# Performance work log

Hardware: AMD Instinct MI355X
Metric: run time of the kernel (lower is better)

The kernel has to match this reference:

```python
import jax, jax.numpy as jnp
import numpy as np

T = 0.2          # temperature
W = 0.1          # loss weight
BIG = 2 ** 30    # sentinel label for masked-out samples


def setup_inputs() -> dict:
    key = jax.random.key(0)
    k1, k2, k3, k4 = jax.random.split(key, 4)
    bs, C, Gn, S = 32, 128, 256, 16
    grouped_features = jax.random.normal(k1, (bs, C, Gn, S), dtype=jnp.float32)
    # instance labels in [-1, 8): -1 = background
    proposal_instance_mask = jax.random.randint(k2, (bs, Gn, S), -1, 8, dtype=jnp.int32)
    # seed indices with duplicates possible (range 40 over 16 samples)
    grouped_indices = jax.random.randint(k3, (bs, Gn, S), 0, 40, dtype=jnp.int32)
    context_compen = jax.random.normal(k4, (1, C), dtype=jnp.float32)
    return {
        "proposal_instance_mask": proposal_instance_mask,
        "grouped_features": grouped_features,
        "grouped_indices": grouped_indices,
        "context_compen": context_compen,
    }


def _group_loss(feat, idx, lab, ctx):
    # feat: [S, C], idx: [S], lab: [S], ctx: [C]
    # NOTE: sum_{a,b} f_a . g_b / (n_f * n_g) == mean(f) . mean(g), so the
    # original tiny-mm contrastive loss reduces to pairwise dots of per-instance means.
    S, C = feat.shape
    pos = jnp.arange(S)
    # unique count of seed indices -> truncate to first u samples (as in torch code)
    si = jnp.sort(idx)
    u = 1 + jnp.sum(si[1:] != si[:-1])
    valid = pos < u
    lab_m = jnp.where(valid, lab, BIG)
    # per-group unique labels (sorted), jit-friendly
    sl = jnp.sort(lab_m)
    new = jnp.concatenate([jnp.ones((1,), bool), sl[1:] != sl[:-1]])
    cid = jnp.cumsum(new) - 1                      # compact id of each sorted label
    uniq = jnp.full((S,), BIG, sl.dtype).at[cid].set(sl)
    n_labels = jnp.sum(new & (sl != BIG))          # number of distinct valid labels
    has_bg = uniq[0] == -1                         # -1 sorts first if present
    # per-instance mean features via segment scatter-add
    comp = jnp.searchsorted(uniq, lab_m)           # sample -> compact instance slot
    sums = jnp.zeros((S, C), feat.dtype).at[comp].add(jnp.where(valid[:, None], feat, 0.0))
    cnts = jnp.zeros((S,), feat.dtype).at[comp].add(valid.astype(feat.dtype))
    means = sums / jnp.maximum(cnts, 1.0)[:, None]
    hb = has_bg.astype(jnp.int32)
    fg_count = n_labels - hb
    inst_num = fg_count + 1                        # bg slot always present
    # row 0 = bg mean (or context_compen if no bg), rows 1.. = fg means
    gidx = jnp.clip(pos + hb - 1, 0, S - 1)
    M = means[gidx]
    M = M.at[0].set(jnp.where(has_bg, M[0], ctx))
    inst_valid = pos < inst_num
    sim = (M @ M.T) / T                            # [S, S] tiny matmul of means
    sim_m = jnp.where(inst_valid[None, :], sim, -jnp.inf)
    lse = jax.scipy.special.logsumexp(sim_m, axis=1)
    li = lse - jnp.diagonal(sim)                   # -log(pos/(pos+neg)) per fg row
    fg_mask = inst_valid & (pos >= 1)
    gl = jnp.sum(jnp.where(fg_mask, li, 0.0)) / jnp.maximum(inst_num - 1, 1).astype(feat.dtype)
    return gl, fg_count >= 1


def reference(proposal_instance_mask, grouped_features, grouped_indices, context_compen):
    bs, C, Gn, S = grouped_features.shape
    feats = grouped_features.transpose(0, 2, 3, 1).reshape(-1, S, C)  # [G, S, C]
    idxs = grouped_indices.reshape(-1, S)
    labs = proposal_instance_mask.reshape(-1, S)
    ctx = context_compen[0]
    gl, gv = jax.vmap(lambda f, i, l: _group_loss(f, i, l, ctx))(feats, idxs, labs)
    gvf = gv.astype(gl.dtype)
    return jnp.sum(gl * gvf) / jnp.sum(gvf) * W
```

## Files before the change

### kernel.cpp

```cpp
#include <hip/hip_runtime.h>

#define GQ   8192
#define WPB  2
#define MROW 132
#define SLICE 1280

__global__ __launch_bounds__(64 * WPB, 6) void group_loss_kernel(
    const int*   __restrict__ labs,
    const float* __restrict__ feats,
    const int*   __restrict__ idxs,
    const float* __restrict__ ctx,
    float2* __restrict__ ws)
{
    __shared__ float SH[WPB * SLICE];

    const int l  = threadIdx.x & 63;
    const int wu = threadIdx.x >> 6;
    float* MM   = SH + wu * SLICE;
    float* SIMM = MM + 9 * MROW;

    const int blk = blockIdx.x;
    const int g  = ((blk & 7) << 10) | ((blk >> 3) << 1) | wu;
    const int b  = g >> 8;
    const int gn = g & 255;
    const long fbase = (long)b * (128 * 256 * 16) + (long)gn * 16;

    const float* gp0 = feats + fbase + (long)l * 4096;
    const float* gp1 = gp0 + 64 * 4096;
    float4 A[4], B[4];
    #pragma unroll
    for (int q = 0; q < 4; ++q) A[q] = *(const float4*)(gp0 + q * 4);
    #pragma unroll
    for (int q = 0; q < 4; ++q) B[q] = *(const float4*)(gp1 + q * 4);
    const float cx0 = ctx[l], cx1 = ctx[l + 64];
    float fa[16], fb[16];
    #pragma unroll
    for (int q = 0; q < 4; ++q) {
        fa[4*q+0] = A[q].x; fa[4*q+1] = A[q].y; fa[4*q+2] = A[q].z; fa[4*q+3] = A[q].w;
        fb[4*q+0] = B[q].x; fb[4*q+1] = B[q].y; fb[4*q+2] = B[q].z; fb[4*q+3] = B[q].w;
    }

    int myidx = -1, mylab = -2;
    if (l < 16) { myidx = idxs[g * 16 + l]; mylab = labs[g * 16 + l]; }

    bool dup = false;
    #pragma unroll
    for (int j = 0; j < 15; ++j) {
        const int vj = __shfl(myidx, j);
        dup = dup || ((l > j) && (myidx == vj));
    }
    const int u = __popcll(__ballot((l < 16) && !dup));

    const bool valid = l < u;
    const int bid = valid ? (mylab + 1) : 255;

    unsigned long long memb[9]; int cnt[9];
    #pragma unroll
    for (int r = 0; r < 9; ++r) {
        memb[r] = __ballot(bid == r);
        cnt[r]  = __popcll(memb[r]);
    }
    const bool has_bg = cnt[0] > 0;
    int fg_count = 0, pm = 0;
    #pragma unroll
    for (int r = 1; r < 9; ++r)
        if (cnt[r] > 0) { ++fg_count; pm |= 1 << r; }

    float m0[9] = {0,0,0,0,0,0,0,0,0};
    float m1[9] = {0,0,0,0,0,0,0,0,0};
    #pragma unroll
    for (int s = 0; s < 16; ++s) {
        if (s < u) {
            const int bs = __builtin_amdgcn_readlane(bid, s);
            switch (bs) {
                case 0: m0[0] += fa[s]; m1[0] += fb[s]; break;
                case 1: m0[1] += fa[s]; m1[1] += fb[s]; break;
                case 2: m0[2] += fa[s]; m1[2] += fb[s]; break;
                case 3: m0[3] += fa[s]; m1[3] += fb[s]; break;
                case 4: m0[4] += fa[s]; m1[4] += fb[s]; break;
                case 5: m0[5] += fa[s]; m1[5] += fb[s]; break;
                case 6: m0[6] += fa[s]; m1[6] += fb[s]; break;
                case 7: m0[7] += fa[s]; m1[7] += fb[s]; break;
                case 8: m0[8] += fa[s]; m1[8] += fb[s]; break;
            }
        }
    }
    #pragma unroll
    for (int r = 0; r < 9; ++r) {
        const float invc = 1.0f / (float)(cnt[r] > 0 ? cnt[r] : 1);
        m0[r] *= invc; m1[r] *= invc;
    }
    if (!has_bg) { m0[0] = cx0; m1[0] = cx1; }

    #pragma unroll
    for (int r = 0; r < 9; ++r) {
        MM[r * MROW + l]      = m0[r];
        MM[r * MROW + 64 + l] = m1[r];
    }
    __syncthreads();

    float simv = 0.0f; int pi = 0, pj = 0;
    if (l < 44) {
        pi = (int)((sqrtf(8.0f * (float)l + 9.0f) - 1.0f) * 0.5f);
        pj = l - (pi * (pi + 1) / 2 - 1);
        const float* Ri = MM + pi * MROW;
        const float* Rj = MM + pj * MROW;
        float acc = 0.0f;
        #pragma unroll
        for (int q = 0; q < 32; ++q) {
            float4 x = *(const float4*)(Ri + 4 * q);
            float4 y = *(const float4*)(Rj + 4 * q);
            acc += x.x * y.x + x.y * y.y + x.z * y.z + x.w * y.w;
        }
        simv = acc * 5.0f;
    }
    if (l < 44) {
        SIMM[pi * 9 + pj] = simv;
        if (pi != pj) SIMM[pj * 9 + pi] = simv;
    }
    __syncthreads();

    float li_val = 0.0f;
    if (l >= 1 && l < 9 && ((pm >> l) & 1)) {
        float srow[9];
        #pragma unroll
        for (int j = 0; j < 9; ++j) srow[j] = SIMM[l * 9 + j];
        float vmax = srow[0];
        #pragma unroll
        for (int j = 1; j < 9; ++j)
            if ((pm >> j) & 1) vmax = fmaxf(vmax, srow[j]);
        float se = __expf(srow[0] - vmax);
        #pragma unroll
        for (int j = 1; j < 9; ++j)
            if ((pm >> j) & 1) se += __expf(srow[j] - vmax);
        li_val = vmax + __logf(se) - srow[l];
    }

    float ssum = li_val;
    #pragma unroll
    for (int off = 8; off >= 1; off >>= 1) ssum += __shfl_down(ssum, off);
    if (l == 0) {
        float2 r;
        r.x = ssum / (float)(fg_count > 0 ? fg_count : 1);
        r.y = (fg_count > 0) ? 1.0f : 0.0f;
        ws[g] = r;
    }
}

__global__ __launch_bounds__(1024) void reduce_kernel(
    const float2* __restrict__ ws, float* __restrict__ out)
{
    __shared__ float sa[1024], sb[1024];
    const int t = threadIdx.x;
    float a = 0.0f, b2 = 0.0f;
    for (int g = t; g < GQ; g += 1024) {
        float2 v = ws[g];
        a += v.x; b2 += v.y;
    }
    sa[t] = a; sb[t] = b2;
    __syncthreads();
    for (int off = 512; off > 0; off >>= 1) {
        if (t < off) { sa[t] += sa[t + off]; sb[t] += sb[t + off]; }
        __syncthreads();
    }
    if (t == 0) out[0] = 0.1f * (sa[0] / sb[0]);
}

extern "C" void kernel_launch(void* const* d_in, const int* in_sizes, int n_in,
                              void* d_out, int out_size, void* d_ws, size_t ws_size,
                              hipStream_t stream) {
    const int*   labs  = (const int*)d_in[0];
    const float* feats = (const float*)d_in[1];
    const int*   idxs  = (const int*)d_in[2];
    const float* ctx   = (const float*)d_in[3];
    float* out = (float*)d_out;
    float2* ws = (float2*)d_ws;

    group_loss_kernel<<<GQ / WPB, 64 * WPB, 0, stream>>>(labs, feats, idxs, ctx, ws);
    reduce_kernel<<<1, 1024, 0, stream>>>(ws, out);
}
```

Measured before the change: 113.4 us.

## Replace shared-memory Gram matrix with DPP wave reductions and bitwise duplicate detection

Drops the LDS staging of per-instance means and the similarity matrix, along with both __syncthreads. Each lane now forms its partial products for all 44 lower-triangle pairs, reduces them across the wave with DPP row and broadcast adds, reads the totals with readlane, and has every lane compute the logsumexp uniformly. Duplicate seed detection switches from 15 shuffles to 6 ballots over index bits, and the sqrt(5) temperature factor is folded into the means. This removes shared-memory traffic and barriers but adds 44 six-step DPP reductions per wave and more registers for pv[44] and svi[44]. The 6-bit index test assumes seed indices stay below 64.

```diff
diff --git a/kernel.cpp b/kernel.cpp
--- a/kernel.cpp
+++ b/kernel.cpp
@@ -2,8 +2,22 @@
 
 #define GQ   8192
 #define WPB  2
-#define MROW 132
-#define SLICE 1280
+#define SQRT5 2.23606797749978969f
+
+template<int CTRL>
+__device__ __forceinline__ float dpp_add(float v) {
+    int t = __builtin_amdgcn_update_dpp(0, __float_as_int(v), CTRL, 0xF, 0xF, true);
+    return v + __int_as_float(t);
+}
+__device__ __forceinline__ float wave_sum64(float v) {
+    v = dpp_add<0x111>(v);
+    v = dpp_add<0x112>(v);
+    v = dpp_add<0x114>(v);
+    v = dpp_add<0x118>(v);
+    v = dpp_add<0x142>(v);
+    v = dpp_add<0x143>(v);
+    return v;
+}
 
 __global__ __launch_bounds__(64 * WPB, 6) void group_loss_kernel(
     const int*   __restrict__ labs,
@@ -12,13 +26,8 @@
     const float* __restrict__ ctx,
     float2* __restrict__ ws)
 {
-    __shared__ float SH[WPB * SLICE];
-
     const int l  = threadIdx.x & 63;
     const int wu = threadIdx.x >> 6;
-    float* MM   = SH + wu * SLICE;
-    float* SIMM = MM + 9 * MROW;
-
     const int blk = blockIdx.x;
     const int g  = ((blk & 7) << 10) | ((blk >> 3) << 1) | wu;
     const int b  = g >> 8;
@@ -33,38 +42,37 @@
     #pragma unroll
     for (int q = 0; q < 4; ++q) B[q] = *(const float4*)(gp1 + q * 4);
     const float cx0 = ctx[l], cx1 = ctx[l + 64];
+
+    int myidx = -1, mylab = -2;
+    if (l < 16) { myidx = idxs[g * 16 + l]; mylab = labs[g * 16 + l]; }
+
+    unsigned long long mm = ~0ull;
+    #pragma unroll
+    for (int bit = 0; bit < 6; ++bit) {
+        const unsigned long long bb = __ballot((myidx >> bit) & 1);
+        mm &= ((myidx >> bit) & 1) ? bb : ~bb;
+    }
+    const bool dup = (mm & ((1ull << l) - 1) & 0xFFFFull) != 0ull;
+    const int u = __popcll(__ballot((l < 16) && !dup));
+
+    const bool valid = l < u;
+    const int bid = valid ? (mylab + 1) : 255;
+
+    int cnt[9];
+    #pragma unroll
+    for (int r = 0; r < 9; ++r) cnt[r] = __popcll(__ballot(bid == r));
+    const bool has_bg = cnt[0] > 0;
+    int fg_count = 0, pm = 0;
+    #pragma unroll
+    for (int r = 1; r < 9; ++r)
+        if (cnt[r] > 0) { ++fg_count; pm |= 1 << r; }
+
     float fa[16], fb[16];
     #pragma unroll
     for (int q = 0; q < 4; ++q) {
         fa[4*q+0] = A[q].x; fa[4*q+1] = A[q].y; fa[4*q+2] = A[q].z; fa[4*q+3] = A[q].w;
         fb[4*q+0] = B[q].x; fb[4*q+1] = B[q].y; fb[4*q+2] = B[q].z; fb[4*q+3] = B[q].w;
     }
-
-    int myidx = -1, mylab = -2;
-    if (l < 16) { myidx = idxs[g * 16 + l]; mylab = labs[g * 16 + l]; }
-
-    bool dup = false;
-    #pragma unroll
-    for (int j = 0; j < 15; ++j) {
-        const int vj = __shfl(myidx, j);
-        dup = dup || ((l > j) && (myidx == vj));
-    }
-    const int u = __popcll(__ballot((l < 16) && !dup));
-
-    const bool valid = l < u;
-    const int bid = valid ? (mylab + 1) : 255;
-
-    unsigned long long memb[9]; int cnt[9];
-    #pragma unroll
-    for (int r = 0; r < 9; ++r) {
-        memb[r] = __ballot(bid == r);
-        cnt[r]  = __popcll(memb[r]);
-    }
-    const bool has_bg = cnt[0] > 0;
-    int fg_count = 0, pm = 0;
-    #pragma unroll
-    for (int r = 1; r < 9; ++r)
-        if (cnt[r] > 0) { ++fg_count; pm |= 1 << r; }
 
     float m0[9] = {0,0,0,0,0,0,0,0,0};
     float m1[9] = {0,0,0,0,0,0,0,0,0};
@@ -87,64 +95,54 @@
     }
     #pragma unroll
     for (int r = 0; r < 9; ++r) {
-        const float invc = 1.0f / (float)(cnt[r] > 0 ? cnt[r] : 1);
-        m0[r] *= invc; m1[r] *= invc;
+        const float sc = SQRT5 / (float)(cnt[r] > 0 ? cnt[r] : 1);
+        m0[r] *= sc; m1[r] *= sc;
     }
-    if (!has_bg) { m0[0] = cx0; m1[0] = cx1; }
+    if (!has_bg) { m0[0] = cx0 * SQRT5; m1[0] = cx1 * SQRT5; }
 
+    const int PI_[44] = {1,1, 2,2,2, 3,3,3,3, 4,4,4,4,4, 5,5,5,5,5,5,
+                         6,6,6,6,6,6,6, 7,7,7,7,7,7,7,7, 8,8,8,8,8,8,8,8,8};
+    const int PJ_[44] = {0,1, 0,1,2, 0,1,2,3, 0,1,2,3,4, 0,1,2,3,4,5,
+                         0,1,2,3,4,5,6, 0,1,2,3,4,5,6,7, 0,1,2,3,4,5,6,7,8};
+    float pv[44];
     #pragma unroll
-    for (int r = 0; r < 9; ++r) {
-        MM[r * MROW + l]      = m0[r];
-        MM[r * MROW + 64 + l] = m1[r];
+    for (int k = 0; k < 44; ++k)
+        pv[k] = m0[PI_[k]] * m0[PJ_[k]] + m1[PI_[k]] * m1[PJ_[k]];
+    #pragma unroll
+    for (int k = 0; k < 44; ++k) pv[k] = wave_sum64(pv[k]);
+
+    const int cm = pm | 1;
+    int svi[44];
+    #pragma unroll
+    for (int k = 0; k < 44; ++k) {
+        const int s = __builtin_amdgcn_readlane(__float_as_int(pv[k]), 63);
+        const bool keep = (((cm >> PI_[k]) & 1) != 0) && (((cm >> PJ_[k]) & 1) != 0);
+        svi[k] = keep ? s : 0xFF800000;
     }
-    __syncthreads();
+    const int OFF_[9] = {0, 0, 2, 5, 9, 14, 20, 27, 35};
+    #define SK(i, j) __int_as_float(svi[((i) >= (j)) ? (OFF_[(i)] + (j)) : (OFF_[(j)] + (i))])
 
-    float simv = 0.0f; int pi = 0, pj = 0;
-    if (l < 44) {
-        pi = (int)((sqrtf(8.0f * (float)l + 9.0f) - 1.0f) * 0.5f);
-        pj = l - (pi * (pi + 1) / 2 - 1);
-        const float* Ri = MM + pi * MROW;
-        const float* Rj = MM + pj * MROW;
-        float acc = 0.0f;
-        #pragma unroll
-        for (int q = 0; q < 32; ++q) {
-            float4 x = *(const float4*)(Ri + 4 * q);
-            float4 y = *(const float4*)(Rj + 4 * q);
-            acc += x.x * y.x + x.y * y.y + x.z * y.z + x.w * y.w;
+    float ssum = 0.0f;
+    #pragma unroll
+    for (int r = 1; r < 9; ++r) {
+        if ((pm >> r) & 1) {
+            float vmax = SK(r, 0);
+            #pragma unroll
+            for (int j = 1; j < 9; ++j) vmax = fmaxf(vmax, SK(r, j));
+            float se = 0.0f;
+            #pragma unroll
+            for (int j = 0; j < 9; ++j) se += __expf(SK(r, j) - vmax);
+            ssum += vmax + __logf(se) - SK(r, r);
         }
-        simv = acc * 5.0f;
-    }
-    if (l < 44) {
-        SIMM[pi * 9 + pj] = simv;
-        if (pi != pj) SIMM[pj * 9 + pi] = simv;
-    }
-    __syncthreads();
-
-    float li_val = 0.0f;
-    if (l >= 1 && l < 9 && ((pm >> l) & 1)) {
-        float srow[9];
-        #pragma unroll
-        for (int j = 0; j < 9; ++j) srow[j] = SIMM[l * 9 + j];
-        float vmax = srow[0];
-        #pragma unroll
-        for (int j = 1; j < 9; ++j)
-            if ((pm >> j) & 1) vmax = fmaxf(vmax, srow[j]);
-        float se = __expf(srow[0] - vmax);
-        #pragma unroll
-        for (int j = 1; j < 9; ++j)
-            if ((pm >> j) & 1) se += __expf(srow[j] - vmax);
-        li_val = vmax + __logf(se) - srow[l];
     }
 
-    float ssum = li_val;
-    #pragma unroll
-    for (int off = 8; off >= 1; off >>= 1) ssum += __shfl_down(ssum, off);
     if (l == 0) {
         float2 r;
         r.x = ssum / (float)(fg_count > 0 ? fg_count : 1);
         r.y = (fg_count > 0) ? 1.0f : 0.0f;
         ws[g] = r;
     }
+    #undef SK
 }
 
 __global__ __launch_bounds__(1024) void reduce_kernel(
```

Measured after the change: 116.1 us. +2.4%, slower.
